# Performance work log

Measured on AMD Instinct MI355X. Metric: run time of the kernel, lower is better.

## Reference

```python
import jax, jax.numpy as jnp
import numpy as np

B, N, M, D0, D, H, KW = 2, 512, 512, 1024, 100, 50, 7
K_SLOPE, X0_SIG = 20.0, 0.5  # LogisticActivation(x0=0.5, k=20), k not trained


def setup_inputs() -> dict:
    key = jax.random.key(0)
    ks = jax.random.split(key, 8)
    s = lambda k, shp: jax.random.normal(k, shp, jnp.float32) * 0.05
    return {
        "x0": jax.random.normal(ks[0], (B, N, D0), jnp.float32),
        "x1": jax.random.normal(ks[1], (B, M, D0), jnp.float32),
        "W_proj": s(ks[2], (D0, D)),
        "b_proj": jnp.zeros((D,), jnp.float32),
        "W_hid": s(ks[3], (2 * D, H)),
        "b_hid": jnp.zeros((H,), jnp.float32),
        "conv_w": s(ks[4], (1, H, KW, KW)),  # OIHW
        "conv_b": jnp.zeros((1,), jnp.float32),
        "theta": jnp.array([0.5], jnp.float32),
        "lambda_": jnp.array([0.3], jnp.float32),
        "gamma": jnp.array([0.2], jnp.float32),
    }


def reference(x0, x1, W_proj, b_proj, W_hid, b_hid, conv_w, conv_b, theta, lambda_, gamma):
    # --- embedding: FullyConnectedEmbed (Linear + ReLU) ---
    e0 = jax.nn.relu(x0 @ W_proj + b_proj)  # [B,N,D]
    e1 = jax.nn.relu(x1 @ W_proj + b_proj)  # [B,M,D]
    # --- contact: broadcast features -> 1x1 conv -> 7x7 conv -> sigmoid ---
    diff = jnp.abs(e0[:, :, None, :] - e1[:, None, :, :])   # [B,N,M,D]
    mul = e0[:, :, None, :] * e1[:, None, :, :]             # [B,N,M,D]
    Z = jnp.concatenate([diff, mul], axis=-1)               # [B,N,M,2D]
    Hh = jax.nn.relu(jnp.einsum('bnmc,ch->bhnm', Z, W_hid) + b_hid[None, :, None, None])
    C = jax.lax.conv_general_dilated(Hh, conv_w, (1, 1), 'SAME')
    C = jax.nn.sigmoid(C + conv_b[None, :, None, None])     # [B,1,N,M]
    # --- weighting matrix W (do_w=True) ---
    i = jnp.arange(N, dtype=jnp.float32)
    j = jnp.arange(M, dtype=jnp.float32)
    a = -jnp.square((i + 1 - (N + 1) / 2) / (-(N + 1) / 2))
    b = -jnp.square((j + 1 - (M + 1) / 2) / (-(M + 1) / 2))
    a = jnp.exp(lambda_ * a)                                 # [N]
    b = jnp.exp(lambda_ * b)                                 # [M]
    W = (1 - theta[0]) * (a[:, None] * b[None, :]) + theta[0]
    yhat = C * W                                             # [B,1,N,M]
    # --- global pooling: mean/var threshold + ratio ---
    mu = jnp.mean(yhat, axis=(1, 2, 3), keepdims=True)
    sigma = jnp.var(yhat, axis=(1, 2, 3), ddof=1, keepdims=True)  # torch.var is unbiased
    Q = jax.nn.relu(yhat - mu - gamma[0] * sigma)
    phat = jnp.sum(Q, axis=(1, 2, 3)) / (jnp.sum(jnp.sign(Q), axis=(1, 2, 3)) + 1)
    # --- LogisticActivation ---
    return jnp.clip(1.0 / (1.0 + jnp.exp(-K_SLOPE * (phat - X0_SIG))), 0.0, 1.0)  # [B]
```

## Files before the change

### kernel.cpp

```cpp
#include <hip/hip_runtime.h>
#include <hip/hip_bf16.h>

static constexpr int Bc   = 2;
static constexpr int Nc   = 512;
static constexpr int Mc   = 512;
static constexpr int D0c  = 1024;
static constexpr int Dc   = 100;
static constexpr int Hc   = 50;
static constexpr long long NMc = (long long)Nc * Mc;

typedef __attribute__((ext_vector_type(8))) short short8v;
typedef __attribute__((ext_vector_type(4))) float f32x4;

__global__ __launch_bounds__(512) void k_embed(
    const float* __restrict__ x0, const float* __restrict__ x1,
    const float* __restrict__ Wp, const float* __restrict__ bp,
    float* __restrict__ e0, float* __restrict__ e1)
{
  __shared__ float xs[8][1024];
  const int t   = threadIdx.x;
  const int rg0 = blockIdx.x * 8;

  #pragma unroll
  for (int i = 0; i < 4; ++i) {
    const int idx = i*512 + t;
    const int r   = idx >> 8;
    const int c4  = idx & 255;
    const int rgs = rg0 + r;
    const float* src = (rgs < Bc*Nc) ? (x0 + (size_t)rgs * D0c)
                                     : (x1 + (size_t)(rgs - Bc*Nc) * D0c);
    *(float4*)&xs[r][c4*4] = *(const float4*)&src[c4*4];
  }
  __syncthreads();

  const int c = t & 127;
  const int q = t >> 7;
  if (c < Dc) {
    const int row0 = q*2, row1 = q*2 + 1;
    float acc0 = 0.f, acc1 = 0.f;
    for (int k = 0; k < D0c; k += 8) {
      float w[8];
      #pragma unroll
      for (int u = 0; u < 8; ++u) w[u] = Wp[(k+u)*Dc + c];
      const float4 xa0 = *(const float4*)&xs[row0][k];
      const float4 xb0 = *(const float4*)&xs[row0][k+4];
      const float4 xa1 = *(const float4*)&xs[row1][k];
      const float4 xb1 = *(const float4*)&xs[row1][k+4];
      acc0 = fmaf(xa0.x, w[0], acc0); acc1 = fmaf(xa1.x, w[0], acc1);
      acc0 = fmaf(xa0.y, w[1], acc0); acc1 = fmaf(xa1.y, w[1], acc1);
      acc0 = fmaf(xa0.z, w[2], acc0); acc1 = fmaf(xa1.z, w[2], acc1);
      acc0 = fmaf(xa0.w, w[3], acc0); acc1 = fmaf(xa1.w, w[3], acc1);
      acc0 = fmaf(xb0.x, w[4], acc0); acc1 = fmaf(xb1.x, w[4], acc1);
      acc0 = fmaf(xb0.y, w[5], acc0); acc1 = fmaf(xb1.y, w[5], acc1);
      acc0 = fmaf(xb0.z, w[6], acc0); acc1 = fmaf(xb1.z, w[6], acc1);
      acc0 = fmaf(xb0.w, w[7], acc0); acc1 = fmaf(xb1.w, w[7], acc1);
    }
    const float bias = bp[c];
    {
      const int rg = rg0 + row0;
      const float v = fmaxf(acc0 + bias, 0.f);
      if (rg < Bc*Nc) e0[(size_t)rg*Dc + c] = v;
      else            e1[(size_t)(rg - Bc*Nc)*Dc + c] = v;
    }
    {
      const int rg = rg0 + row1;
      const float v = fmaxf(acc1 + bias, 0.f);
      if (rg < Bc*Nc) e0[(size_t)rg*Dc + c] = v;
      else            e1[(size_t)(rg - Bc*Nc)*Dc + c] = v;
    }
  }
}

__global__ __launch_bounds__(64) void k_wsplit(
    const float* __restrict__ Whid, uint4* __restrict__ wsplit)
{
  const int fi = blockIdx.x;
  const int s  = fi >> 3;
  const int ht = (fi >> 1) & 3;
  const int hl = fi & 1;
  const int lane = threadIdx.x;
  const int h_loc = lane & 15, g = lane >> 4;
  const int h = ht*16 + h_loc;
  uint dw[4] = {0u,0u,0u,0u};
  #pragma unroll
  for (int j = 0; j < 8; ++j) {
    const int p = j >> 2, q = j & 3;
    const int d = s*16 + g*4 + q;
    float wv = (h < Hc && d < Dc) ? Whid[(size_t)(p*Dc + d)*Hc + h] : 0.f;
    const uint bits = __float_as_uint(wv);
    const uint hi_bits = bits & 0xffff0000u;
    uint e16;
    if (hl == 0) e16 = hi_bits >> 16;
    else {
      const float lo = wv - __uint_as_float(hi_bits);
      e16 = __float_as_uint(lo) >> 16;
    }
    dw[j >> 1] |= e16 << (16 * (j & 1));
  }
  uint4 v; v.x = dw[0]; v.y = dw[1]; v.z = dw[2]; v.w = dw[3];
  wsplit[fi*64 + lane] = v;
}

__global__ __launch_bounds__(256) void k_hh(
    const float* __restrict__ e0, const float* __restrict__ e1,
    const uint4* __restrict__ wsplit, const float* __restrict__ bhid,
    float* __restrict__ hh, int slab_n0, int slabh)
{
  const int b  = blockIdx.z;
  const int lr = blockIdx.y;
  const int n  = slab_n0 + lr;
  if ((unsigned)n >= (unsigned)Nc) return;

  __shared__ float e1T[32][112];
  __shared__ float e0s[112];
  __shared__ float biasl[64];
  __shared__ float ldsC[4][2][16][17];

  const int t   = threadIdx.x;
  const int m0b = blockIdx.x * 32;

  for (int i = t; i < 32*112; i += 256) {
    const int row = i / 112, col = i - row*112;
    e1T[row][col] = (col < Dc) ? e1[((size_t)(b*Mc + m0b + row))*Dc + col] : 0.f;
  }
  if (t < 112) e0s[t] = (t < Dc) ? e0[((size_t)(b*Nc + n))*Dc + t] : 0.f;
  if (t >= 128 && t < 192) { const int h = t - 128; biasl[h] = (h < Hc) ? bhid[h] : 0.f; }
  __syncthreads();

  const int w = t >> 6, lane = t & 63;
  const int cl = lane & 15, g = lane >> 4;
  const int mt = w >> 1;
  const int hhalf = w & 1;

  f32x4 c0 = {0.f,0.f,0.f,0.f}, c1 = {0.f,0.f,0.f,0.f};

  union U { uint4 u; short8v v; };

  for (int s = 0; s < 7; ++s) {
    const int d0 = s*16 + g*4;
    const float4 E1 = *(const float4*)&e1T[mt*16 + cl][d0];
    const float4 E0 = *(const float4*)&e0s[d0];

    const float df0 = fabsf(E0.x - E1.x), df1 = fabsf(E0.y - E1.y),
                df2 = fabsf(E0.z - E1.z), df3 = fabsf(E0.w - E1.w);
    const float pm0 = E0.x*E1.x, pm1 = E0.y*E1.y,
                pm2 = E0.z*E1.z, pm3 = E0.w*E1.w;

    #define PK(a,bq) ((__float_as_uint(bq) & 0xffff0000u) | (__float_as_uint(a) >> 16))
    #define LO(x) ((x) - __uint_as_float(__float_as_uint(x) & 0xffff0000u))
    U ahi, alo;
    ahi.u.x = PK(df0, df1); ahi.u.y = PK(df2, df3);
    ahi.u.z = PK(pm0, pm1); ahi.u.w = PK(pm2, pm3);
    const float l0 = LO(df0), l1 = LO(df1), l2 = LO(df2), l3 = LO(df3);
    const float l4 = LO(pm0), l5 = LO(pm1), l6 = LO(pm2), l7 = LO(pm3);
    alo.u.x = PK(l0, l1); alo.u.y = PK(l2, l3);
    alo.u.z = PK(l4, l5); alo.u.w = PK(l6, l7);
    #undef PK
    #undef LO

    const int ht0 = hhalf*2, ht1 = hhalf*2 + 1;
    U whi0, wlo0, whi1, wlo1;
    whi0.u = wsplit[((s*4 + ht0)*2 + 0)*64 + lane];
    wlo0.u = wsplit[((s*4 + ht0)*2 + 1)*64 + lane];
    whi1.u = wsplit[((s*4 + ht1)*2 + 0)*64 + lane];
    wlo1.u = wsplit[((s*4 + ht1)*2 + 1)*64 + lane];

    c0 = __builtin_amdgcn_mfma_f32_16x16x32_bf16(ahi.v, whi0.v, c0, 0, 0, 0);
    c0 = __builtin_amdgcn_mfma_f32_16x16x32_bf16(alo.v, whi0.v, c0, 0, 0, 0);
    c0 = __builtin_amdgcn_mfma_f32_16x16x32_bf16(ahi.v, wlo0.v, c0, 0, 0, 0);
    c1 = __builtin_amdgcn_mfma_f32_16x16x32_bf16(ahi.v, whi1.v, c1, 0, 0, 0);
    c1 = __builtin_amdgcn_mfma_f32_16x16x32_bf16(alo.v, whi1.v, c1, 0, 0, 0);
    c1 = __builtin_amdgcn_mfma_f32_16x16x32_bf16(ahi.v, wlo1.v, c1, 0, 0, 0);
  }

  #pragma unroll
  for (int r = 0; r < 4; ++r) {
    ldsC[w][0][cl][g*4 + r] = c0[r];
    ldsC[w][1][cl][g*4 + r] = c1[r];
  }

  #pragma unroll
  for (int pass = 0; pass < 8; ++pass) {
    const int row   = pass*4 + g;
    const int tile  = row >> 4, hl2 = row & 15;
    const int h     = (hhalf*2 + tile)*16 + hl2;
    if (h < Hc) {
      float v = ldsC[w][tile][hl2][cl] + biasl[h];
      v = fmaxf(v, 0.f);
      hh[(((size_t)(b*Hc + h))*slabh + lr)*Mc + (m0b + mt*16 + cl)] = v;
    }
  }
}

__global__ __launch_bounds__(256) void k_conv(
    const float* __restrict__ hh, const float* __restrict__ cw,
    const float* __restrict__ cb, const float* __restrict__ theta,
    const float* __restrict__ lam, float* __restrict__ yhat,
    double* __restrict__ gacc, int n_begin, int slabh)
{
  __shared__ float tile[2][38*40];
  __shared__ double red[2][4];
  const int t  = threadIdx.x;
  const int b  = blockIdx.z;
  const int n0 = n_begin + blockIdx.y * 32;
  const int m0 = blockIdx.x * 32;

  const int rr = t >> 3;
  const int c0 = 4 * (t & 7);

  float stg[6];
  auto issue = [&](int h) {
    #pragma unroll
    for (int it = 0; it < 6; ++it) {
      const int idx = it*256 + t;
      float v = 0.f;
      if (idx < 38*38) {
        const int r = idx / 38, c = idx - r*38;
        const int gn = n0 - 3 + r, gm = m0 - 3 + c;
        if ((unsigned)gn < (unsigned)Nc && (unsigned)gm < (unsigned)Mc)
          v = hh[(((size_t)(b*Hc + h))*slabh + (gn - n_begin + 3))*Mc + gm];
      }
      stg[it] = v;
    }
  };
  auto commit = [&](int buf) {
    #pragma unroll
    for (int it = 0; it < 6; ++it) {
      const int idx = it*256 + t;
      if (idx < 38*38) {
        const int r = idx / 38, c = idx - r*38;
        tile[buf][r*40 + c] = stg[it];
      }
    }
  };

  issue(0); commit(0);
  __syncthreads();

  float acc0 = 0.f, acc1 = 0.f, acc2 = 0.f, acc3 = 0.f;
  for (int h = 0; h < Hc; ++h) {
    if (h + 1 < Hc) issue(h + 1);
    const int buf = h & 1;
    const float* __restrict__ cp = cw + h*49;
    #pragma unroll
    for (int dn = 0; dn < 7; ++dn) {
      const float* tp = &tile[buf][(rr+dn)*40 + c0];
      const float4 wa = *(const float4*)tp;
      const float4 wb = *(const float4*)(tp+4);
      const float2 wc = *(const float2*)(tp+8);
      const float w_[10] = {wa.x,wa.y,wa.z,wa.w, wb.x,wb.y,wb.z,wb.w, wc.x,wc.y};
      #pragma unroll
      for (int dm = 0; dm < 7; ++dm) {
        const float wv = cp[dn*7 + dm];
        acc0 = fmaf(w_[dm],   wv, acc0);
        acc1 = fmaf(w_[dm+1], wv, acc1);
        acc2 = fmaf(w_[dm+2], wv, acc2);
        acc3 = fmaf(w_[dm+3], wv, acc3);
      }
    }
    __syncthreads();
    if (h + 1 < Hc) { commit((h+1) & 1); __syncthreads(); }
  }

  const float th  = theta[0];
  const float lm  = lam[0];
  const float cbv = cb[0];
  const int n = n0 + rr;
  const int m = m0 + c0;
  const float half1 = 0.5f * (float)(Nc + 1);
  const float inv   = 1.0f / half1;
  const float ti  = ((float)(n+1) - half1) * inv;
  const float av  = expf(-lm * ti * ti);
  float y[4];
  double s = 0.0, ss = 0.0;
  const float a_[4] = {acc0, acc1, acc2, acc3};
  #pragma unroll
  for (int j = 0; j < 4; ++j) {
    const float tj = ((float)(m+1+j) - half1) * inv;
    const float bv = expf(-lm * tj * tj);
    const float sg = 1.f / (1.f + expf(-(a_[j] + cbv)));
    y[j] = sg * ((1.f - th) * av * bv + th);
    s  += (double)y[j];
    ss += (double)y[j] * (double)y[j];
  }
  float4 yv; yv.x = y[0]; yv.y = y[1]; yv.z = y[2]; yv.w = y[3];
  *(float4*)&yhat[((size_t)(b*Nc + n))*Mc + m] = yv;

  for (int off = 32; off > 0; off >>= 1) {
    s  += __shfl_down(s,  off);
    ss += __shfl_down(ss, off);
  }
  const int wave = t >> 6, lane = t & 63;
  if (lane == 0) { red[0][wave] = s; red[1][wave] = ss; }
  __syncthreads();
  if (t == 0) {
    atomicAdd(&gacc[b*4 + 0], red[0][0] + red[0][1] + red[0][2] + red[0][3]);
    atomicAdd(&gacc[b*4 + 1], red[1][0] + red[1][1] + red[1][2] + red[1][3]);
  }
}

__global__ __launch_bounds__(256) void k_q(
    const float* __restrict__ yhat, double* __restrict__ gacc,
    const float* __restrict__ gamma)
{
  const int tid = blockIdx.x * 256 + threadIdx.x;
  const int b = blockIdx.x >> 8;
  const float4 y = ((const float4*)yhat)[tid];
  const double sum = gacc[b*4 + 0], ssq = gacc[b*4 + 1];
  const double mu  = sum / (double)NMc;
  const double var = (ssq - sum * mu) / ((double)NMc - 1.0);
  const double thr = mu + (double)gamma[0] * var;

  double sq = 0.0; int c = 0;
  double q;
  q = (double)y.x - thr; if (q > 0.0) { sq += q; ++c; }
  q = (double)y.y - thr; if (q > 0.0) { sq += q; ++c; }
  q = (double)y.z - thr; if (q > 0.0) { sq += q; ++c; }
  q = (double)y.w - thr; if (q > 0.0) { sq += q; ++c; }

  for (int off = 32; off > 0; off >>= 1) {
    sq += __shfl_down(sq, off);
    c  += __shfl_down(c,  off);
  }
  __shared__ double sr[4];
  __shared__ int    cr[4];
  const int wave = threadIdx.x >> 6, lane = threadIdx.x & 63;
  if (lane == 0) { sr[wave] = sq; cr[wave] = c; }
  __syncthreads();
  if (threadIdx.x == 0) {
    atomicAdd(&gacc[b*4 + 2], sr[0] + sr[1] + sr[2] + sr[3]);
    atomicAdd(&gacc[b*4 + 3], (double)(cr[0] + cr[1] + cr[2] + cr[3]));
  }
}

__global__ void k_out(const double* __restrict__ gacc, float* __restrict__ out)
{
  const int t = threadIdx.x;
  if (t < Bc) {
    const double phat = gacc[t*4 + 2] / (gacc[t*4 + 3] + 1.0);
    double v = 1.0 / (1.0 + exp(-20.0 * (phat - 0.5)));
    v = fmin(fmax(v, 0.0), 1.0);
    out[t] = (float)v;
  }
}

extern "C" void kernel_launch(void* const* d_in, const int* in_sizes, int n_in,
                              void* d_out, int out_size, void* d_ws, size_t ws_size,
                              hipStream_t stream)
{
  const float* x0 = (const float*)d_in[0];
  const float* x1 = (const float*)d_in[1];
  const float* Wp = (const float*)d_in[2];
  const float* bp = (const float*)d_in[3];
  const float* Wh = (const float*)d_in[4];
  const float* bh = (const float*)d_in[5];
  const float* cw = (const float*)d_in[6];
  const float* cb = (const float*)d_in[7];
  const float* th = (const float*)d_in[8];
  const float* lm = (const float*)d_in[9];
  const float* gm = (const float*)d_in[10];
  float* out = (float*)d_out;
  (void)in_sizes; (void)n_in; (void)out_size;

  int slabrows, nslab;
  if      (ws_size >= (size_t)109232128) { slabrows = 512; nslab = 1; }
  else if (ws_size >= (size_t)56803328)  { slabrows = 256; nslab = 2; }
  else                                    { slabrows = 128; nslab = 4; }
  const int slabh = slabrows + 6;
  const size_t hh_bytes = (size_t)slabh * 204800;

  char* ws = (char*)d_ws;
  float*  e0   = (float*)(ws);
  float*  e1   = (float*)(ws + 409600);
  double* gacc = (double*)(ws + 819200);
  uint4*  wsp  = (uint4*)(ws + 884736);
  float*  hh   = (float*)(ws + 1048576);
  float*  yhat = (float*)(ws + 1048576 + hh_bytes);

  hipMemsetAsync(gacc, 0, 64, stream);
  k_wsplit<<<dim3(56), dim3(64), 0, stream>>>(Wh, wsp);
  k_embed<<<dim3(256), dim3(512), 0, stream>>>(x0, x1, Wp, bp, e0, e1);
  for (int s = 0; s < nslab; ++s) {
    const int n_begin = s * slabrows;
    k_hh  <<<dim3(16, slabh, 2), dim3(256), 0, stream>>>(
        e0, e1, wsp, bh, hh, n_begin - 3, slabh);
    k_conv<<<dim3(16, slabrows / 32, 2), dim3(256), 0, stream>>>(
        hh, cw, cb, th, lm, yhat, gacc, n_begin, slabh);
  }
  k_q  <<<dim3(512), dim3(256), 0, stream>>>(yhat, gacc, gm);
  k_out<<<dim3(1),   dim3(64),  0, stream>>>(gacc, out);
}
```

Measured before the change: 302.5 us.

## Restructure k_hh to compute two rows per block and drop a conv barrier

Each k_hh block now covers two n-rows and 32 m-columns. Each wave computes all four hidden-unit MFMA tiles, which halves the grid and reuses each e1 tile and W-split fragment across more work. The e1 tile is loaded with float4 accesses, bf16 hi/lo packing uses a byte-permute intrinsic, and the epilogue goes through a smaller per-wave LDS transpose. A redundant __syncthreads in the double-buffered conv loop is removed. In exchange, each wave holds more accumulator registers (launch bounds now 256,4), and the barrier removal depends on the buffer-reuse pattern staying race-free.

```diff
diff --git a/kernel.cpp b/kernel.cpp
--- a/kernel.cpp
+++ b/kernel.cpp
@@ -11,6 +11,13 @@
 
 typedef __attribute__((ext_vector_type(8))) short short8v;
 typedef __attribute__((ext_vector_type(4))) float f32x4;
+
+__device__ __forceinline__ unsigned pk_hi(float a, float b) {
+  return __builtin_amdgcn_perm(__float_as_uint(b), __float_as_uint(a), 0x07060302u);
+}
+__device__ __forceinline__ float trunc16(float x) {
+  return __uint_as_float(__float_as_uint(x) & 0xffff0000u);
+}
 
 __global__ __launch_bounds__(512) void k_embed(
     const float* __restrict__ x0, const float* __restrict__ x1,
@@ -101,93 +108,112 @@
   wsplit[fi*64 + lane] = v;
 }
 
-__global__ __launch_bounds__(256) void k_hh(
+__global__ __launch_bounds__(256, 4) void k_hh(
     const float* __restrict__ e0, const float* __restrict__ e1,
     const uint4* __restrict__ wsplit, const float* __restrict__ bhid,
     float* __restrict__ hh, int slab_n0, int slabh)
 {
-  const int b  = blockIdx.z;
-  const int lr = blockIdx.y;
-  const int n  = slab_n0 + lr;
-  if ((unsigned)n >= (unsigned)Nc) return;
-
-  __shared__ float e1T[32][112];
-  __shared__ float e0s[112];
+  const int b   = blockIdx.z;
+  const int lr0 = blockIdx.y * 2;
+  const int n0base = slab_n0 + lr0;
+  if (n0base + 1 < 0 || n0base >= Nc) return;
+
+  __shared__ float e1T[32][116];
+  __shared__ float e0s[2][112];
   __shared__ float biasl[64];
-  __shared__ float ldsC[4][2][16][17];
+  __shared__ float ldsT[4][16][17];
 
   const int t   = threadIdx.x;
   const int m0b = blockIdx.x * 32;
 
-  for (int i = t; i < 32*112; i += 256) {
-    const int row = i / 112, col = i - row*112;
-    e1T[row][col] = (col < Dc) ? e1[((size_t)(b*Mc + m0b + row))*Dc + col] : 0.f;
-  }
-  if (t < 112) e0s[t] = (t < Dc) ? e0[((size_t)(b*Nc + n))*Dc + t] : 0.f;
-  if (t >= 128 && t < 192) { const int h = t - 128; biasl[h] = (h < Hc) ? bhid[h] : 0.f; }
+  {
+    const int row = t >> 3;
+    const int cb  = (t & 7) * 4;
+    const float* src = e1 + (size_t)(b*Mc + m0b + row) * Dc;
+    #pragma unroll
+    for (int pass = 0; pass < 4; ++pass) {
+      const int col = cb + pass*32;
+      if (col < 112) {
+        float4 v = {0.f,0.f,0.f,0.f};
+        if (col < Dc) v = *(const float4*)&src[col];
+        *(float4*)&e1T[row][col] = v;
+      }
+    }
+  }
+  {
+    const int nl2 = t >> 7, col = t & 127;
+    if (col < 112) {
+      const int n = n0base + nl2;
+      float v = 0.f;
+      if ((unsigned)n < (unsigned)Nc && col < Dc)
+        v = e0[(size_t)(b*Nc + n)*Dc + col];
+      e0s[nl2][col] = v;
+    }
+  }
+  if (t < 64) biasl[t] = (t < Hc) ? bhid[t] : 0.f;
   __syncthreads();
 
   const int w = t >> 6, lane = t & 63;
   const int cl = lane & 15, g = lane >> 4;
-  const int mt = w >> 1;
-  const int hhalf = w & 1;
-
-  f32x4 c0 = {0.f,0.f,0.f,0.f}, c1 = {0.f,0.f,0.f,0.f};
+  const int nl   = w >> 1;
+  const int mrow = (w & 1) * 16 + cl;
+
+  f32x4 acc0 = {0.f,0.f,0.f,0.f}, acc1 = {0.f,0.f,0.f,0.f};
+  f32x4 acc2 = {0.f,0.f,0.f,0.f}, acc3 = {0.f,0.f,0.f,0.f};
 
   union U { uint4 u; short8v v; };
-
+  const uint4* __restrict__ wq = wsplit + lane;
+
+  #pragma unroll
   for (int s = 0; s < 7; ++s) {
     const int d0 = s*16 + g*4;
-    const float4 E1 = *(const float4*)&e1T[mt*16 + cl][d0];
-    const float4 E0 = *(const float4*)&e0s[d0];
+    const float4 E1 = *(const float4*)&e1T[mrow][d0];
+    const float4 E0 = *(const float4*)&e0s[nl][d0];
 
     const float df0 = fabsf(E0.x - E1.x), df1 = fabsf(E0.y - E1.y),
                 df2 = fabsf(E0.z - E1.z), df3 = fabsf(E0.w - E1.w);
     const float pm0 = E0.x*E1.x, pm1 = E0.y*E1.y,
                 pm2 = E0.z*E1.z, pm3 = E0.w*E1.w;
 
-    #define PK(a,bq) ((__float_as_uint(bq) & 0xffff0000u) | (__float_as_uint(a) >> 16))
-    #define LO(x) ((x) - __uint_as_float(__float_as_uint(x) & 0xffff0000u))
     U ahi, alo;
-    ahi.u.x = PK(df0, df1); ahi.u.y = PK(df2, df3);
-    ahi.u.z = PK(pm0, pm1); ahi.u.w = PK(pm2, pm3);
-    const float l0 = LO(df0), l1 = LO(df1), l2 = LO(df2), l3 = LO(df3);
-    const float l4 = LO(pm0), l5 = LO(pm1), l6 = LO(pm2), l7 = LO(pm3);
-    alo.u.x = PK(l0, l1); alo.u.y = PK(l2, l3);
-    alo.u.z = PK(l4, l5); alo.u.w = PK(l6, l7);
-    #undef PK
-    #undef LO
-
-    const int ht0 = hhalf*2, ht1 = hhalf*2 + 1;
-    U whi0, wlo0, whi1, wlo1;
-    whi0.u = wsplit[((s*4 + ht0)*2 + 0)*64 + lane];
-    wlo0.u = wsplit[((s*4 + ht0)*2 + 1)*64 + lane];
-    whi1.u = wsplit[((s*4 + ht1)*2 + 0)*64 + lane];
-    wlo1.u = wsplit[((s*4 + ht1)*2 + 1)*64 + lane];
-
-    c0 = __builtin_amdgcn_mfma_f32_16x16x32_bf16(ahi.v, whi0.v, c0, 0, 0, 0);
-    c0 = __builtin_amdgcn_mfma_f32_16x16x32_bf16(alo.v, whi0.v, c0, 0, 0, 0);
-    c0 = __builtin_amdgcn_mfma_f32_16x16x32_bf16(ahi.v, wlo0.v, c0, 0, 0, 0);
-    c1 = __builtin_amdgcn_mfma_f32_16x16x32_bf16(ahi.v, whi1.v, c1, 0, 0, 0);
-    c1 = __builtin_amdgcn_mfma_f32_16x16x32_bf16(alo.v, whi1.v, c1, 0, 0, 0);
-    c1 = __builtin_amdgcn_mfma_f32_16x16x32_bf16(ahi.v, wlo1.v, c1, 0, 0, 0);
-  }
-
+    ahi.u.x = pk_hi(df0, df1); ahi.u.y = pk_hi(df2, df3);
+    ahi.u.z = pk_hi(pm0, pm1); ahi.u.w = pk_hi(pm2, pm3);
+    alo.u.x = pk_hi(df0 - trunc16(df0), df1 - trunc16(df1));
+    alo.u.y = pk_hi(df2 - trunc16(df2), df3 - trunc16(df3));
+    alo.u.z = pk_hi(pm0 - trunc16(pm0), pm1 - trunc16(pm1));
+    alo.u.w = pk_hi(pm2 - trunc16(pm2), pm3 - trunc16(pm3));
+
+    #pragma unroll
+    for (int ht = 0; ht < 4; ++ht) {
+      U whi, wlo;
+      whi.u = wq[((s*4 + ht)*2 + 0)*64];
+      wlo.u = wq[((s*4 + ht)*2 + 1)*64];
+      f32x4* ac = (ht == 0) ? &acc0 : (ht == 1) ? &acc1 : (ht == 2) ? &acc2 : &acc3;
+      *ac = __builtin_amdgcn_mfma_f32_16x16x32_bf16(ahi.v, whi.v, *ac, 0, 0, 0);
+      *ac = __builtin_amdgcn_mfma_f32_16x16x32_bf16(alo.v, whi.v, *ac, 0, 0, 0);
+      *ac = __builtin_amdgcn_mfma_f32_16x16x32_bf16(ahi.v, wlo.v, *ac, 0, 0, 0);
+    }
+  }
+
+  const int n = n0base + nl;
+  const bool nvalid = (unsigned)n < (unsigned)Nc;
+  const int S = slabh * Mc;
+  float* hhp = hh + ((size_t)b*Hc)*S + (size_t)(lr0 + nl)*Mc
+                  + (m0b + (w & 1)*16 + cl) + (size_t)g*S;
+
+  const f32x4 accs[4] = {acc0, acc1, acc2, acc3};
   #pragma unroll
-  for (int r = 0; r < 4; ++r) {
-    ldsC[w][0][cl][g*4 + r] = c0[r];
-    ldsC[w][1][cl][g*4 + r] = c1[r];
-  }
-
-  #pragma unroll
-  for (int pass = 0; pass < 8; ++pass) {
-    const int row   = pass*4 + g;
-    const int tile  = row >> 4, hl2 = row & 15;
-    const int h     = (hhalf*2 + tile)*16 + hl2;
-    if (h < Hc) {
-      float v = ldsC[w][tile][hl2][cl] + biasl[h];
-      v = fmaxf(v, 0.f);
-      hh[(((size_t)(b*Hc + h))*slabh + lr)*Mc + (m0b + mt*16 + cl)] = v;
+  for (int ht = 0; ht < 4; ++ht) {
+    #pragma unroll
+    for (int r = 0; r < 4; ++r) ldsT[w][cl][g*4 + r] = accs[ht][r];
+    #pragma unroll
+    for (int p = 0; p < 4; ++p) {
+      const int hl2 = p*4 + g;
+      const int h = ht*16 + hl2;
+      if (h < Hc && nvalid) {
+        const float v = fmaxf(ldsT[w][hl2][cl] + biasl[h], 0.f);
+        hhp[(size_t)((ht*16 + p*4) * S)] = v;
+      }
     }
   }
 }
@@ -258,7 +284,6 @@
         acc3 = fmaf(w_[dm+3], wv, acc3);
       }
     }
-    __syncthreads();
     if (h + 1 < Hc) { commit((h+1) & 1); __syncthreads(); }
   }
 
@@ -382,7 +407,7 @@
   k_embed<<<dim3(256), dim3(512), 0, stream>>>(x0, x1, Wp, bp, e0, e1);
   for (int s = 0; s < nslab; ++s) {
     const int n_begin = s * slabrows;
-    k_hh  <<<dim3(16, slabh, 2), dim3(256), 0, stream>>>(
+    k_hh  <<<dim3(16, slabh/2, 2), dim3(256), 0, stream>>>(
         e0, e1, wsp, bh, hh, n_begin - 3, slabh);
     k_conv<<<dim3(16, slabrows / 32, 2), dim3(256), 0, stream>>>(
         hh, cw, cb, th, lm, yhat, gacc, n_begin, slabh);
```

Result: faster. 283.7 us (-6.2%).
